# Performance work log

Measured on AMD Instinct MI355X. Metric: run time of the kernel, lower is better.

The kernel has to match this reference:

```python
import jax, jax.numpy as jnp
import numpy as np
from jax import lax

L, BSZ, H, W, U, P = 16, 8, 32, 32, 128, 256
KB = KC = KD = 3
NUM_GROUPS = 32
DT_MIN, DT_MAX = 1e-3, 1e-1
EPS = 1e-5


def setup_inputs() -> dict:
    key = jax.random.key(0)
    ks = jax.random.split(key, 10)
    return {
        "input_sequence": jax.random.normal(ks[0], (L, BSZ, H, W, U), jnp.float32),
        "x0": jax.random.normal(ks[1], (BSZ, H, W, P), jnp.float32),
        # negative real parts of continuous-time eigenvalues
        "Lambda_re": -(0.5 * jax.random.uniform(ks[2], (P,), jnp.float32) + 1e-2),
        "Lambda_im": jax.random.normal(ks[3], (P,), jnp.float32) * jnp.pi,
        # B param (P,U,kB,kB,2) real/imag stacked (he-normal scale)
        "B_ri": jax.random.normal(ks[4], (P, U, KB, KB, 2), jnp.float32) / np.sqrt(U * KB * KB),
        # C param (U,P,kC,kC,2) real/imag stacked
        "C_ri": jax.random.normal(ks[5], (U, P, KC, KC, 2), jnp.float32) / np.sqrt(P * KC * KC),
        "log_step": jax.random.uniform(ks[6], (P,), jnp.float32) * (np.log(DT_MAX) - np.log(DT_MIN)) + np.log(DT_MIN),
        # diagonal (depthwise) feedthrough D conv kernel, HWIO with I=1
        "D_kernel": jax.random.normal(ks[7], (KD, KD, 1, U), jnp.float32) / KD,
        "gn_scale": jnp.ones((U,), jnp.float32),
        "gn_bias": jnp.zeros((U,), jnp.float32),
    }


def _conv(x, k):
    # x: (N,H,W,Cin), k: (kh,kw,Cin,Cout), SAME padding, stride 1
    return lax.conv_general_dilated(x, k, (1, 1), 'SAME',
                                    dimension_numbers=('NHWC', 'HWIO', 'NHWC'))


def _group_norm(x, scale, bias):
    n, h, w, c = x.shape
    xg = x.reshape(n, h, w, NUM_GROUPS, c // NUM_GROUPS)
    mu = xg.mean(axis=(1, 2, 4), keepdims=True)
    var = xg.var(axis=(1, 2, 4), keepdims=True)
    xg = (xg - mu) * lax.rsqrt(var + EPS)
    return xg.reshape(n, h, w, c) * scale + bias


def reference(input_sequence, x0, Lambda_re, Lambda_im, B_ri, C_ri, log_step,
              D_kernel, gn_scale, gn_bias):
    # ---- discretization (faithful to source discretize_zoh: A_bar = Lambda*Delta, B_bar = Delta*B_tilde) ----
    Lam = jnp.minimum(Lambda_re, -1e-4) + 1j * Lambda_im      # clip_eigs, (P,) complex64
    step = jnp.exp(log_step)                                   # (P,)
    A_bar = Lam * step                                         # (P,) complex64
    # B_bar = (1/Lambda)*Lambda_bar*B_tilde = Delta * B_tilde, laid out HWIO (kB,kB,U,P)
    Bk_r = jnp.transpose(B_ri[..., 0] * step[:, None, None, None], (2, 3, 1, 0))
    Bk_i = jnp.transpose(B_ri[..., 1] * step[:, None, None, None], (2, 3, 1, 0))
    # C_tilde kernel HWIO (kC,kC,P,U)
    Ck_r = jnp.transpose(C_ri[..., 0], (2, 3, 1, 0))
    Ck_i = jnp.transpose(C_ri[..., 1], (2, 3, 1, 0))

    # ---- B (*) u for all timesteps (fold L into batch) ----
    u = input_sequence.reshape(L * BSZ, H, W, U)
    Bus = (_conv(u, Bk_r) + 1j * _conv(u, Bk_i)).reshape(L, BSZ, H, W, P)  # complex64
    Bus = Bus.at[0].add(A_bar * x0.astype(Bus.dtype))

    # ---- diagonal parallel scan: x_k = A * x_{k-1} + (B (*) u_k) ----
    A_elems = jnp.broadcast_to(A_bar[None, None, None, None, :], (L, 1, 1, 1, P))

    def binop(qi, qj):
        Ai, bi = qi
        Aj, bj = qj
        return Aj * Ai, Aj * bi + bj

    _, xs = lax.associative_scan(binop, (A_elems, Bus))        # xs: (L,BSZ,H,W,P) complex

    # ---- ys = 2*Re(C (*) x) ----
    xr = xs.real.reshape(L * BSZ, H, W, P)
    xi = xs.imag.reshape(L * BSZ, H, W, P)
    ys = 2.0 * (_conv(xr, Ck_r) - _conv(xi, Ck_i))             # (L*BSZ,H,W,U)

    # ---- C_D conv head ('standard' Diag_CD_Conv): diagonal D feedthrough + GroupNorm + act ----
    Du = lax.conv_general_dilated(u, D_kernel, (1, 1), 'SAME',
                                  dimension_numbers=('NHWC', 'HWIO', 'NHWC'),
                                  feature_group_count=U)
    h = jax.nn.gelu(_group_norm(ys + Du, gn_scale, gn_bias))
    ys_out = h.reshape(L, BSZ, H, W, U)

    x_last = xs[-1]                                            # (BSZ,H,W,P) complex
    x_last_ri = jnp.stack([x_last.real, x_last.imag], axis=-1) # real view for harness
    return x_last_ri, ys_out
```

## Files before the change

kernel.cpp:

```cpp
#include <hip/hip_runtime.h>
#include <hip/hip_bf16.h>
#include <math.h>

#define Ldim 16
#define BATCH 8
#define HWdim 1024

typedef __attribute__((ext_vector_type(8))) short s8v;
typedef __attribute__((ext_vector_type(4))) short s4v;
typedef __attribute__((ext_vector_type(2))) short s2v;
typedef __attribute__((ext_vector_type(4))) float f32x4;
typedef __attribute__((ext_vector_type(2))) float f32x2;

__device__ __forceinline__ short f2bf(float f) {
    __hip_bfloat16 h = __float2bfloat16(f);
    return __builtin_bit_cast(short, h);
}
__device__ __forceinline__ float bf2f(short s) {
    __hip_bfloat16 h = __builtin_bit_cast(__hip_bfloat16, s);
    return __bfloat162float(h);
}

__device__ __forceinline__ void gload_lds16(const short* g, short* l) {
    __builtin_amdgcn_global_load_lds(
        (const __attribute__((address_space(1))) void*)g,
        (__attribute__((address_space(3))) void*)l, 16, 0, 0);
}

__global__ __launch_bounds__(256)
void prep_kernel(const float* __restrict__ Lre, const float* __restrict__ Lim,
                 const float* __restrict__ B_ri, const float* __restrict__ C_ri,
                 const float* __restrict__ log_step, short* __restrict__ Wb,
                 short* __restrict__ Wc, float* __restrict__ Abar) {
    int tid = blockIdx.x * 256 + threadIdx.x;
    if (tid < 256) {
        float st = expf(log_step[tid]);
        Abar[tid] = fminf(Lre[tid], -1e-4f) * st;
        Abar[256 + tid] = Lim[tid] * st;
    }
    const int total = 9 * 512 * 128;
    for (int i = tid; i < total; i += gridDim.x * 256) {
        int tile = i >> 13;
        int r = i & 8191;
        int A = r * 2;
        int cout_lc = A >> 7;
        int remb = A & 127;
        int ci2 = remb ^ ((cout_lc & 7) << 4);
        int ci_local = ci2 >> 1;
        {
            int cgp = tile / 18;
            int rm = tile % 18;
            int ch = rm / 9, t = rm % 9;
            int cout = cgp * 128 + cout_lc;
            int p = cout >> 1, ri = cout & 1;
            int u = ch * 64 + ci_local;
            float val = B_ri[(((size_t)p * 128 + u) * 9 + t) * 2 + ri] * expf(log_step[p]);
            Wb[i] = f2bf(val);
        }
        {
            int ch = tile / 9;
            int t = tile % 9;
            int u = cout_lc;
            int k = ch * 64 + ci_local;
            int p = k >> 1, ri = k & 1;
            float val = C_ri[(((size_t)u * 256 + p) * 9 + t) * 2 + ri];
            val = ri ? -2.f * val : 2.f * val;
            Wc[i] = f2bf(val);
        }
    }
}

__global__ __launch_bounds__(256)
void ubf_slice_kernel(const float* __restrict__ u, short* __restrict__ Ubf,
                      int b0, int Gshift) {
    size_t t = (size_t)blockIdx.x * 256 + threadIdx.x;
    int c8 = (int)(t & 15);
    int hw = (int)(t >> 4) & 1023;
    int img = (int)(t >> 14);
    int l = img >> Gshift, bi = img & ((1 << Gshift) - 1);
    const float* src = u + (((size_t)(l * BATCH + b0 + bi) * HWdim + hw) * 128 + c8 * 8);
    f32x4 v0 = *(const f32x4*)src;
    f32x4 v1 = *(const f32x4*)(src + 4);
    s8v o;
#pragma unroll
    for (int j = 0; j < 4; ++j) { o[j] = f2bf(v0[j]); o[4 + j] = f2bf(v1[j]); }
    *(s8v*)(Ubf + ((size_t)img * HWdim + hw) * 128 + c8 * 8) = o;
}

template <int CIN, int COUT, bool INF32, bool INFULL, bool RMW>
__global__ __launch_bounds__(256, 2)
void conv_mfma(const void* __restrict__ inbuf, const short* __restrict__ Wt,
               short* __restrict__ outbuf, int b0, int Gshift) {
    constexpr int NCH = CIN / 64;
    constexpr int NT = NCH * 9;
    constexpr int NCGP = COUT / 128;
    __shared__ short ilds[6 * 34 * 64];
    __shared__ short wlds[3 * 8192];

    const int tid = threadIdx.x;
    const int lane = tid & 63;
    const int wv = tid >> 6;
    const int waveM = wv & 1, waveN = wv >> 1;
    const int lm = lane & 15, quad = lane >> 4;

    const int chunk = gridDim.x >> 3;
    const int wg = blockIdx.x;
    const int wgs = (wg & 7) * chunk + (wg >> 3);
    const int cgp = wgs % NCGP;
    const int h0 = (((wgs / NCGP) & 7)) * 4;
    const int img = wgs / (NCGP * 8);

    const int l = img >> Gshift;
    const int bi = img & ((1 << Gshift) - 1);
    const size_t inframe = INFULL ? (size_t)(l * BATCH + b0 + bi) : (size_t)img;

    constexpr int NST = 7;
    uint goff[NST];
    int laddr[NST];
#pragma unroll
    for (int j = 0; j < NST; ++j) {
        int idx = tid + j * 256;
        laddr[j] = -1;
        goff[j] = 0xFFFFFFFFu;
        if (idx < 6 * 34 * 8) {
            int cgi = idx & 7;
            int pos = idx >> 3;
            int w34 = pos % 34;
            int sr = pos / 34;
            int habs = h0 - 1 + sr, wabs = w34 - 1;
            laddr[j] = ((pos << 3) + (cgi ^ (pos & 7))) << 3;
            if ((unsigned)habs < 32u && (unsigned)wabs < 32u)
                goff[j] = (uint)(((uint)inframe * HWdim + habs * 32 + wabs) * CIN + cgi * 8);
        }
    }

    auto issue_W = [&](int j) {
        const short* src = Wt + ((size_t)cgp * NT + j) * 8192;
        short* dst = &wlds[(j % 3) * 8192];
#pragma unroll
        for (int r = 0; r < 4; ++r)
            gload_lds16(src + (size_t)(r * 256 + tid) * 8, dst + (r * 256 + wv * 64) * 8);
    };

    auto stage_input = [&](int ch) {
        s8v sreg[NST];
#pragma unroll
        for (int j = 0; j < NST; ++j) {
            s8v v = (s8v){0, 0, 0, 0, 0, 0, 0, 0};
            if (goff[j] != 0xFFFFFFFFu) {
                if constexpr (INF32) {
                    const float* src = (const float*)inbuf + goff[j] + ch * 64;
                    f32x4 a0 = *(const f32x4*)src;
                    f32x4 a1 = *(const f32x4*)(src + 4);
#pragma unroll
                    for (int q = 0; q < 4; ++q) { v[q] = f2bf(a0[q]); v[4 + q] = f2bf(a1[q]); }
                } else {
                    v = *(const s8v*)((const short*)inbuf + goff[j] + ch * 64);
                }
            }
            sreg[j] = v;
        }
#pragma unroll
        for (int j = 0; j < NST; ++j)
            if (laddr[j] >= 0) *(s8v*)&ilds[laddr[j]] = sreg[j];
    };

    f32x4 acc[4][4];
#pragma unroll
    for (int mt = 0; mt < 4; ++mt)
#pragma unroll
        for (int nt = 0; nt < 4; ++nt)
            acc[mt][nt] = (f32x4){0.f, 0.f, 0.f, 0.f};

    auto compute_tap = [&](int t, const short* wb) {
        int kh = t / 3, kw = t - kh * 3;
#pragma unroll
        for (int ks = 0; ks < 2; ++ks) {
            s8v a[4], b[4];
#pragma unroll
            for (int mt = 0; mt < 4; ++mt) {
                int p = (waveM * 2 + (mt >> 1) + kh) * 34 + (mt & 1) * 16 + lm + kw;
                int c = ks * 4 + quad;
                a[mt] = *(const s8v*)&ilds[(((p << 3) + (c ^ (p & 7))) << 3)];
            }
#pragma unroll
            for (int nt = 0; nt < 4; ++nt) {
                int cl = waveN * 64 + nt * 16 + lm;
                int ba = (cl * 128 + ks * 64 + quad * 16) ^ ((cl & 7) << 4);
                b[nt] = *(const s8v*)((const char*)wb + ba);
            }
            __builtin_amdgcn_s_setprio(1);
#pragma unroll
            for (int mt = 0; mt < 4; ++mt)
#pragma unroll
                for (int nt = 0; nt < 4; ++nt)
                    acc[mt][nt] = __builtin_amdgcn_mfma_f32_16x16x32_bf16(
                        b[nt], a[mt], acc[mt][nt], 0, 0, 0);
            __builtin_amdgcn_s_setprio(0);
        }
    };

    issue_W(0);
    if (NT > 1) issue_W(1);
    stage_input(0);
    asm volatile("s_waitcnt vmcnt(0) lgkmcnt(0)" ::: "memory");
    __builtin_amdgcn_sched_barrier(0);
    __builtin_amdgcn_s_barrier();

#pragma unroll
    for (int k = 0; k < NT; ++k) {
        const int ch = k / 9;
        const int t = k - ch * 9;
        if (k + 2 < NT) issue_W(k + 2);
        compute_tap(t, &wlds[(k % 3) * 8192]);
        if (k + 1 < NT) {
            if (k + 2 < NT) {
                asm volatile("s_waitcnt vmcnt(4)" ::: "memory");
            } else {
                asm volatile("s_waitcnt vmcnt(0)" ::: "memory");
            }
            __builtin_amdgcn_sched_barrier(0);
            __builtin_amdgcn_s_barrier();
            if (t == 8) {
                stage_input(ch + 1);
                asm volatile("s_waitcnt lgkmcnt(0)" ::: "memory");
                __builtin_amdgcn_sched_barrier(0);
                __builtin_amdgcn_s_barrier();
            }
        }
    }

#pragma unroll
    for (int mt = 0; mt < 4; ++mt) {
        int px = waveM * 64 + mt * 16 + lm;
        int r = px >> 5, w = px & 31;
        size_t rowbase = ((size_t)img * HWdim + (h0 + r) * 32 + w) * COUT +
                         cgp * 128 + waveN * 64 + quad * 4;
#pragma unroll
        for (int nt = 0; nt < 4; ++nt) {
            size_t oidx = rowbase + nt * 16;
            s4v o;
            if (RMW) {
                s4v old = *(const s4v*)&outbuf[oidx];
#pragma unroll
                for (int reg = 0; reg < 4; ++reg)
                    o[reg] = f2bf(acc[mt][nt][reg] + bf2f(old[reg]));
            } else {
#pragma unroll
                for (int reg = 0; reg < 4; ++reg)
                    o[reg] = f2bf(acc[mt][nt][reg]);
            }
            *(s4v*)&outbuf[oidx] = o;
        }
    }
}

__global__ __launch_bounds__(256)
void scan_kernel(const float* __restrict__ x0, const float* __restrict__ Abar,
                 short* __restrict__ X, float* __restrict__ out_xlast, int b0, int G) {
    int p = threadIdx.x;
    int hw = blockIdx.x;
    int bi = blockIdx.y;
    int b = b0 + bi;
    float Ar = Abar[p], Ai = Abar[256 + p];
    float xr = x0[((size_t)b * HWdim + hw) * 256 + p];
    float xi = 0.f;
    for (int l = 0; l < Ldim; ++l) {
        size_t base = ((size_t)(l * G + bi) * HWdim + hw) * 512 + p * 2;
        s2v v = *(s2v*)&X[base];
        float br = bf2f(v[0]), bim = bf2f(v[1]);
        float nr = Ar * xr - Ai * xi + br;
        float ni = Ar * xi + Ai * xr + bim;
        xr = nr; xi = ni;
        v[0] = f2bf(xr); v[1] = f2bf(xi);
        *(s2v*)&X[base] = v;
    }
    f32x2 o2 = {xr, xi};
    *(f32x2*)&out_xlast[(((size_t)b * HWdim + hw) * 256 + p) * 2] = o2;
}

template <bool UBF>
__global__ __launch_bounds__(256)
void du_kernel(const void* __restrict__ uin, const float* __restrict__ Dk,
               short* __restrict__ ys, int b0, int Gshift) {
    int tid = blockIdx.x * 256 + threadIdx.x;
    int c4 = tid & 31;
    int hw = (tid >> 5) & 1023;
    int img = tid >> 15;
    int h = hw >> 5, w = hw & 31;
    int l = img >> Gshift, bi = img & ((1 << Gshift) - 1);
    size_t fbase = UBF ? (size_t)img * HWdim * 128
                       : ((size_t)(l * BATCH + b0 + bi)) * HWdim * 128;
    float s0 = 0.f, s1 = 0.f, s2 = 0.f, s3 = 0.f;
#pragma unroll
    for (int kh = 0; kh < 3; ++kh)
#pragma unroll
        for (int kw = 0; kw < 3; ++kw) {
            int hh = h + kh - 1, wc = w + kw - 1;
            if ((unsigned)hh < 32u && (unsigned)wc < 32u) {
                f32x4 d = *(const f32x4*)&Dk[(kh * 3 + kw) * 128 + c4 * 4];
                size_t off = fbase + ((size_t)hh * 32 + wc) * 128 + c4 * 4;
                if (UBF) {
                    s4v v = *(const s4v*)((const short*)uin + off);
                    s0 += bf2f(v[0]) * d[0]; s1 += bf2f(v[1]) * d[1];
                    s2 += bf2f(v[2]) * d[2]; s3 += bf2f(v[3]) * d[3];
                } else {
                    f32x4 v = *(const f32x4*)((const float*)uin + off);
                    s0 += v[0] * d[0]; s1 += v[1] * d[1];
                    s2 += v[2] * d[2]; s3 += v[3] * d[3];
                }
            }
        }
    s4v o = {f2bf(s0), f2bf(s1), f2bf(s2), f2bf(s3)};
    *(s4v*)&ys[(size_t)tid * 4] = o;
}

__global__ __launch_bounds__(256)
void gnstats_kernel(const short* __restrict__ ys, float* __restrict__ stats) {
    int g = blockIdx.x;
    int img = blockIdx.y;
    int tid = threadIdx.x;
    float s = 0.f, s2 = 0.f;
    for (int hw = tid; hw < HWdim; hw += 256) {
        s4v v = *(const s4v*)&ys[((size_t)img * HWdim + hw) * 128 + g * 4];
#pragma unroll
        for (int j = 0; j < 4; ++j) {
            float f = bf2f(v[j]);
            s += f; s2 += f * f;
        }
    }
    __shared__ float red[16];
    for (int off = 32; off > 0; off >>= 1) {
        s += __shfl_down(s, off, 64);
        s2 += __shfl_down(s2, off, 64);
    }
    int wid = tid >> 6;
    if ((tid & 63) == 0) { red[wid] = s; red[8 + wid] = s2; }
    __syncthreads();
    if (tid == 0) {
        float S = 0.f, S2 = 0.f;
        for (int w2 = 0; w2 < 4; ++w2) { S += red[w2]; S2 += red[8 + w2]; }
        const float inv = 1.f / (HWdim * 4);
        float mean = S * inv;
        float var = S2 * inv - mean * mean;
        stats[(img * 32 + g) * 2 + 0] = mean;
        stats[(img * 32 + g) * 2 + 1] = var;
    }
}

__global__ __launch_bounds__(256)
void gnapply_kernel(const short* __restrict__ ys, const float* __restrict__ stats,
                    const float* __restrict__ scale, const float* __restrict__ bias,
                    float* __restrict__ out_ys, int b0, int Gshift) {
    int tid = blockIdx.x * 256 + threadIdx.x;
    int c4 = tid & 31;
    int hw = (tid >> 5) & 1023;
    int img = tid >> 15;
    int l = img >> Gshift, bi = img & ((1 << Gshift) - 1);
    float mean = stats[(img * 32 + c4) * 2 + 0];
    float var = stats[(img * 32 + c4) * 2 + 1];
    float rstd = rsqrtf(var + 1e-5f);
    s4v v = *(const s4v*)&ys[(size_t)tid * 4];
    f32x4 sc = *(const f32x4*)&scale[c4 * 4];
    f32x4 bs = *(const f32x4*)&bias[c4 * 4];
    f32x4 o;
    const float kAlpha = 0.7978845608028654f;
#pragma unroll
    for (int j = 0; j < 4; ++j) {
        float y = (bf2f(v[j]) - mean) * rstd * sc[j] + bs[j];
        float t = kAlpha * (y + 0.044715f * y * y * y);
        o[j] = 0.5f * y * (1.f + tanhf(t));
    }
    *(f32x4*)&out_ys[(((size_t)(l * BATCH + b0 + bi)) * HWdim + hw) * 128 + c4 * 4] = o;
}

extern "C" void kernel_launch(void* const* d_in, const int* in_sizes, int n_in,
                              void* d_out, int out_size, void* d_ws, size_t ws_size,
                              hipStream_t stream) {
    const float* useq = (const float*)d_in[0];
    const float* x0 = (const float*)d_in[1];
    const float* Lre = (const float*)d_in[2];
    const float* Lim = (const float*)d_in[3];
    const float* B_ri = (const float*)d_in[4];
    const float* C_ri = (const float*)d_in[5];
    const float* log_step = (const float*)d_in[6];
    const float* Dk = (const float*)d_in[7];
    const float* gsc = (const float*)d_in[8];
    const float* gbi = (const float*)d_in[9];
    float* out = (float*)d_out;

    const size_t WBYTES = 9 * 512 * 128 * 2;

    int G = 2;
    bool ubf = false;
    {
        auto need = [&](int g, bool u) -> size_t {
            size_t base = 2 * WBYTES + 2048 + (size_t)g * 4096;
            size_t x = (size_t)g * Ldim * HWdim * 512 * 2;
            size_t ysb = (size_t)g * Ldim * HWdim * 128 * 2;
            size_t ub = (size_t)g * Ldim * HWdim * 128 * 2;
            return base + x + ysb + (u ? ub : 0);
        };
        if (ws_size >= need(8, true)) { G = 8; ubf = true; }
        else if (ws_size >= need(8, false)) { G = 8; }
        else if (ws_size >= need(4, true)) { G = 4; ubf = true; }
        else if (ws_size >= need(4, false)) { G = 4; }
        else if (ws_size >= need(2, true)) { G = 2; ubf = true; }
    }
    int Gshift = (G == 8) ? 3 : (G == 4) ? 2 : 1;
    int imgs = Ldim * G;

    char* wsb = (char*)d_ws;
    short* Wb = (short*)(wsb);
    short* Wc = (short*)(wsb + WBYTES);
    float* Abar = (float*)(wsb + 2 * WBYTES);
    float* stats = (float*)(wsb + 2 * WBYTES + 2048);
    size_t offX = 2 * WBYTES + 2048 + (size_t)G * 4096;
    short* X = (short*)(wsb + offX);
    size_t offYS = offX + (size_t)G * Ldim * HWdim * 512 * 2;
    short* YS = (short*)(wsb + offYS);
    short* Ubf = (short*)(wsb + offYS + (size_t)G * Ldim * HWdim * 128 * 2);

    prep_kernel<<<2304, 256, 0, stream>>>(Lre, Lim, B_ri, C_ri, log_step, Wb, Wc, Abar);

    for (int b0 = 0; b0 < BATCH; b0 += G) {
        if (ubf) {
            ubf_slice_kernel<<<imgs * 64, 256, 0, stream>>>(useq, Ubf, b0, Gshift);
            conv_mfma<128, 512, false, false, false><<<8 * 4 * imgs, 256, 0, stream>>>(
                Ubf, Wb, X, b0, Gshift);
        } else {
            conv_mfma<128, 512, true, true, false><<<8 * 4 * imgs, 256, 0, stream>>>(
                useq, Wb, X, b0, Gshift);
        }
        scan_kernel<<<dim3(HWdim, G), 256, 0, stream>>>(x0, Abar, X, out, b0, G);
        if (ubf)
            du_kernel<true><<<imgs * 128, 256, 0, stream>>>(Ubf, Dk, YS, b0, Gshift);
        else
            du_kernel<false><<<imgs * 128, 256, 0, stream>>>(useq, Dk, YS, b0, Gshift);
        conv_mfma<512, 128, false, false, true><<<8 * imgs, 256, 0, stream>>>(
            X, Wc, YS, b0, Gshift);
        gnstats_kernel<<<dim3(32, imgs), 256, 0, stream>>>(YS, stats);
        gnapply_kernel<<<imgs * 128, 256, 0, stream>>>(YS, stats, gsc, gbi, out + 4194304, b0,
                                                       Gshift);
    }
}
```

Baseline: 609.6 us.

## Split weight tiles into K-halves, templatize row tile, nontemporal stores

Repacks the B and C conv weights into half-size tiles, one per 32-channel K-step, so the LDS weight ring is halved and the pipeline advances per K-half. The conv kernel gains a row-tile template parameter. The C conv (512->128) now uses 2-row tiles with twice as many workgroups, and launch bounds rise to 3 waves per SIMD for higher occupancy. Nontemporal loads and stores are added in the scan, the conv output and the GN apply to reduce cache pollution. The trade-off is more barriers per tap and lower reuse per tile in the C conv.

```diff
diff --git a/kernel.cpp b/kernel.cpp
--- a/kernel.cpp
+++ b/kernel.cpp
@@ -40,28 +40,29 @@
     }
     const int total = 9 * 512 * 128;
     for (int i = tid; i < total; i += gridDim.x * 256) {
-        int tile = i >> 13;
-        int r = i & 8191;
-        int A = r * 2;
-        int cout_lc = A >> 7;
-        int remb = A & 127;
-        int ci2 = remb ^ ((cout_lc & 7) << 4);
-        int ci_local = ci2 >> 1;
+        int j = i >> 12;
+        int L = (i & 4095) * 2;
+        int c1 = L >> 7;
+        int c0 = ((L >> 6) ^ (L >> 8)) & 1;
+        int cout_lc = c1 * 2 + c0;
+        int cih = ((L ^ ((cout_lc & 7) << 4)) >> 1) & 31;
+        int ks = j & 1;
+        int tt = j >> 1;
         {
-            int cgp = tile / 18;
-            int rm = tile % 18;
+            int cgp = tt / 18;
+            int rm = tt % 18;
             int ch = rm / 9, t = rm % 9;
             int cout = cgp * 128 + cout_lc;
             int p = cout >> 1, ri = cout & 1;
-            int u = ch * 64 + ci_local;
+            int u = ch * 64 + ks * 32 + cih;
             float val = B_ri[(((size_t)p * 128 + u) * 9 + t) * 2 + ri] * expf(log_step[p]);
             Wb[i] = f2bf(val);
         }
         {
-            int ch = tile / 9;
-            int t = tile % 9;
+            int ch = tt / 9;
+            int t = tt % 9;
             int u = cout_lc;
-            int k = ch * 64 + ci_local;
+            int k = ch * 64 + ks * 32 + cih;
             int p = k >> 1, ri = k & 1;
             float val = C_ri[(((size_t)u * 256 + p) * 9 + t) * 2 + ri];
             val = ri ? -2.f * val : 2.f * val;
@@ -87,15 +88,18 @@
     *(s8v*)(Ubf + ((size_t)img * HWdim + hw) * 128 + c8 * 8) = o;
 }
 
-template <int CIN, int COUT, bool INF32, bool INFULL, bool RMW>
-__global__ __launch_bounds__(256, 2)
+template <int TM, int CIN, int COUT, bool INF32, bool INFULL, bool RMW>
+__global__ __launch_bounds__(256, 3)
 void conv_mfma(const void* __restrict__ inbuf, const short* __restrict__ Wt,
                short* __restrict__ outbuf, int b0, int Gshift) {
     constexpr int NCH = CIN / 64;
     constexpr int NT = NCH * 9;
     constexpr int NCGP = COUT / 128;
-    __shared__ short ilds[6 * 34 * 64];
-    __shared__ short wlds[3 * 8192];
+    constexpr int NRG = 32 / TM;
+    constexpr int PR = TM + 2;
+    constexpr int NST = (PR * 34 * 8 + 255) / 256;
+    __shared__ short ilds[PR * 34 * 64];
+    __shared__ short wlds[3 * 4096];
 
     const int tid = threadIdx.x;
     const int lane = tid & 63;
@@ -107,14 +111,13 @@
     const int wg = blockIdx.x;
     const int wgs = (wg & 7) * chunk + (wg >> 3);
     const int cgp = wgs % NCGP;
-    const int h0 = (((wgs / NCGP) & 7)) * 4;
-    const int img = wgs / (NCGP * 8);
+    const int h0 = ((wgs / NCGP) % NRG) * TM;
+    const int img = wgs / (NCGP * NRG);
 
     const int l = img >> Gshift;
     const int bi = img & ((1 << Gshift) - 1);
     const size_t inframe = INFULL ? (size_t)(l * BATCH + b0 + bi) : (size_t)img;
 
-    constexpr int NST = 7;
     uint goff[NST];
     int laddr[NST];
 #pragma unroll
@@ -122,7 +125,7 @@
         int idx = tid + j * 256;
         laddr[j] = -1;
         goff[j] = 0xFFFFFFFFu;
-        if (idx < 6 * 34 * 8) {
+        if (idx < PR * 34 * 8) {
             int cgi = idx & 7;
             int pos = idx >> 3;
             int w34 = pos % 34;
@@ -134,11 +137,11 @@
         }
     }
 
-    auto issue_W = [&](int j) {
-        const short* src = Wt + ((size_t)cgp * NT + j) * 8192;
-        short* dst = &wlds[(j % 3) * 8192];
-#pragma unroll
-        for (int r = 0; r < 4; ++r)
+    auto issue_half = [&](int j, int slot) {
+        const short* src = Wt + ((size_t)cgp * (2 * NT) + j) * 4096;
+        short* dst = &wlds[slot * 4096];
+#pragma unroll
+        for (int r = 0; r < 2; ++r)
             gload_lds16(src + (size_t)(r * 256 + tid) * 8, dst + (r * 256 + wv * 64) * 8);
     };
 
@@ -165,74 +168,80 @@
             if (laddr[j] >= 0) *(s8v*)&ilds[laddr[j]] = sreg[j];
     };
 
-    f32x4 acc[4][4];
-#pragma unroll
-    for (int mt = 0; mt < 4; ++mt)
+    f32x4 acc[TM][4];
+#pragma unroll
+    for (int mt = 0; mt < TM; ++mt)
 #pragma unroll
         for (int nt = 0; nt < 4; ++nt)
             acc[mt][nt] = (f32x4){0.f, 0.f, 0.f, 0.f};
 
-    auto compute_tap = [&](int t, const short* wb) {
-        int kh = t / 3, kw = t - kh * 3;
-#pragma unroll
-        for (int ks = 0; ks < 2; ++ks) {
-            s8v a[4], b[4];
-#pragma unroll
-            for (int mt = 0; mt < 4; ++mt) {
-                int p = (waveM * 2 + (mt >> 1) + kh) * 34 + (mt & 1) * 16 + lm + kw;
-                int c = ks * 4 + quad;
-                a[mt] = *(const s8v*)&ilds[(((p << 3) + (c ^ (p & 7))) << 3)];
-            }
-#pragma unroll
-            for (int nt = 0; nt < 4; ++nt) {
-                int cl = waveN * 64 + nt * 16 + lm;
-                int ba = (cl * 128 + ks * 64 + quad * 16) ^ ((cl & 7) << 4);
-                b[nt] = *(const s8v*)((const char*)wb + ba);
-            }
-            __builtin_amdgcn_s_setprio(1);
-#pragma unroll
-            for (int mt = 0; mt < 4; ++mt)
-#pragma unroll
-                for (int nt = 0; nt < 4; ++nt)
-                    acc[mt][nt] = __builtin_amdgcn_mfma_f32_16x16x32_bf16(
-                        b[nt], a[mt], acc[mt][nt], 0, 0, 0);
-            __builtin_amdgcn_s_setprio(0);
-        }
+    auto compute_ks = [&](int kh, int kw, int ks, int slot) {
+        const char* wb = (const char*)wlds + slot * 8192;
+        s8v a[TM], b[4];
+#pragma unroll
+        for (int mt = 0; mt < TM; ++mt) {
+            int pxb = waveM * (TM * 16) + mt * 16;
+            int p = ((pxb >> 5) + kh) * 34 + (pxb & 31) + lm + kw;
+            int c = ks * 4 + quad;
+            a[mt] = *(const s8v*)&ilds[(((p << 3) + (c ^ (p & 7))) << 3)];
+        }
+#pragma unroll
+        for (int nt = 0; nt < 4; ++nt) {
+            int cl = waveN * 64 + nt * 16 + lm;
+            int ba = (cl * 64 + quad * 16) ^ ((cl & 7) << 4);
+            b[nt] = *(const s8v*)(wb + ba);
+        }
+        __builtin_amdgcn_s_setprio(1);
+#pragma unroll
+        for (int mt = 0; mt < TM; ++mt)
+#pragma unroll
+            for (int nt = 0; nt < 4; ++nt)
+                acc[mt][nt] = __builtin_amdgcn_mfma_f32_16x16x32_bf16(
+                    b[nt], a[mt], acc[mt][nt], 0, 0, 0);
+        __builtin_amdgcn_s_setprio(0);
     };
 
-    issue_W(0);
-    if (NT > 1) issue_W(1);
+    issue_half(0, 0);
+    issue_half(1, 1);
     stage_input(0);
     asm volatile("s_waitcnt vmcnt(0) lgkmcnt(0)" ::: "memory");
     __builtin_amdgcn_sched_barrier(0);
     __builtin_amdgcn_s_barrier();
 
-#pragma unroll
-    for (int k = 0; k < NT; ++k) {
-        const int ch = k / 9;
-        const int t = k - ch * 9;
-        if (k + 2 < NT) issue_W(k + 2);
-        compute_tap(t, &wlds[(k % 3) * 8192]);
-        if (k + 1 < NT) {
-            if (k + 2 < NT) {
-                asm volatile("s_waitcnt vmcnt(4)" ::: "memory");
-            } else {
-                asm volatile("s_waitcnt vmcnt(0)" ::: "memory");
+#pragma unroll 1
+    for (int ch = 0; ch < NCH; ++ch) {
+#pragma unroll
+        for (int t = 0; t < 9; ++t) {
+            const int kh = t / 3, kw = t - kh * 3;
+#pragma unroll
+            for (int ks = 0; ks < 2; ++ks) {
+                const int ls = t * 2 + ks;
+                const int jg = ch * 18 + ls + 2;
+                if (jg < 2 * NT) issue_half(jg, (ls + 2) % 3);
+                compute_ks(kh, kw, ks, ls % 3);
+                const bool last = (ch == NCH - 1) && (ls == 17);
+                if (!last) {
+                    if (jg < 2 * NT) {
+                        asm volatile("s_waitcnt vmcnt(2)" ::: "memory");
+                    } else {
+                        asm volatile("s_waitcnt vmcnt(0)" ::: "memory");
+                    }
+                    __builtin_amdgcn_sched_barrier(0);
+                    __builtin_amdgcn_s_barrier();
+                    if (ls == 17) {
+                        stage_input(ch + 1);
+                        asm volatile("s_waitcnt lgkmcnt(0)" ::: "memory");
+                        __builtin_amdgcn_sched_barrier(0);
+                        __builtin_amdgcn_s_barrier();
+                    }
+                }
             }
-            __builtin_amdgcn_sched_barrier(0);
-            __builtin_amdgcn_s_barrier();
-            if (t == 8) {
-                stage_input(ch + 1);
-                asm volatile("s_waitcnt lgkmcnt(0)" ::: "memory");
-                __builtin_amdgcn_sched_barrier(0);
-                __builtin_amdgcn_s_barrier();
-            }
-        }
-    }
-
-#pragma unroll
-    for (int mt = 0; mt < 4; ++mt) {
-        int px = waveM * 64 + mt * 16 + lm;
+        }
+    }
+
+#pragma unroll
+    for (int mt = 0; mt < TM; ++mt) {
+        int px = waveM * (TM * 16) + mt * 16 + lm;
         int r = px >> 5, w = px & 31;
         size_t rowbase = ((size_t)img * HWdim + (h0 + r) * 32 + w) * COUT +
                          cgp * 128 + waveN * 64 + quad * 4;
@@ -245,12 +254,13 @@
 #pragma unroll
                 for (int reg = 0; reg < 4; ++reg)
                     o[reg] = f2bf(acc[mt][nt][reg] + bf2f(old[reg]));
+                *(s4v*)&outbuf[oidx] = o;
             } else {
 #pragma unroll
                 for (int reg = 0; reg < 4; ++reg)
                     o[reg] = f2bf(acc[mt][nt][reg]);
+                __builtin_nontemporal_store(o, (s4v*)&outbuf[oidx]);
             }
-            *(s4v*)&outbuf[oidx] = o;
         }
     }
 }
@@ -267,7 +277,7 @@
     float xi = 0.f;
     for (int l = 0; l < Ldim; ++l) {
         size_t base = ((size_t)(l * G + bi) * HWdim + hw) * 512 + p * 2;
-        s2v v = *(s2v*)&X[base];
+        s2v v = __builtin_nontemporal_load((const s2v*)&X[base]);
         float br = bf2f(v[0]), bim = bf2f(v[1]);
         float nr = Ar * xr - Ai * xi + br;
         float ni = Ar * xi + Ai * xr + bim;
@@ -276,7 +286,7 @@
         *(s2v*)&X[base] = v;
     }
     f32x2 o2 = {xr, xi};
-    *(f32x2*)&out_xlast[(((size_t)b * HWdim + hw) * 256 + p) * 2] = o2;
+    __builtin_nontemporal_store(o2, (f32x2*)&out_xlast[(((size_t)b * HWdim + hw) * 256 + p) * 2]);
 }
 
 template <bool UBF>
@@ -371,7 +381,8 @@
         float t = kAlpha * (y + 0.044715f * y * y * y);
         o[j] = 0.5f * y * (1.f + tanhf(t));
     }
-    *(f32x4*)&out_ys[(((size_t)(l * BATCH + b0 + bi)) * HWdim + hw) * 128 + c4 * 4] = o;
+    __builtin_nontemporal_store(
+        o, (f32x4*)&out_ys[(((size_t)(l * BATCH + b0 + bi)) * HWdim + hw) * 128 + c4 * 4]);
 }
 
 extern "C" void kernel_launch(void* const* d_in, const int* in_sizes, int n_in,
@@ -426,10 +437,10 @@
     for (int b0 = 0; b0 < BATCH; b0 += G) {
         if (ubf) {
             ubf_slice_kernel<<<imgs * 64, 256, 0, stream>>>(useq, Ubf, b0, Gshift);
-            conv_mfma<128, 512, false, false, false><<<8 * 4 * imgs, 256, 0, stream>>>(
+            conv_mfma<4, 128, 512, false, false, false><<<8 * 4 * imgs, 256, 0, stream>>>(
                 Ubf, Wb, X, b0, Gshift);
         } else {
-            conv_mfma<128, 512, true, true, false><<<8 * 4 * imgs, 256, 0, stream>>>(
+            conv_mfma<4, 128, 512, true, true, false><<<8 * 4 * imgs, 256, 0, stream>>>(
                 useq, Wb, X, b0, Gshift);
         }
         scan_kernel<<<dim3(HWdim, G), 256, 0, stream>>>(x0, Abar, X, out, b0, G);
@@ -437,7 +448,7 @@
             du_kernel<true><<<imgs * 128, 256, 0, stream>>>(Ubf, Dk, YS, b0, Gshift);
         else
             du_kernel<false><<<imgs * 128, 256, 0, stream>>>(useq, Dk, YS, b0, Gshift);
-        conv_mfma<512, 128, false, false, true><<<8 * imgs, 256, 0, stream>>>(
+        conv_mfma<2, 512, 128, false, false, true><<<16 * imgs, 256, 0, stream>>>(
             X, Wc, YS, b0, Gshift);
         gnstats_kernel<<<dim3(32, imgs), 256, 0, stream>>>(YS, stats);
         gnapply_kernel<<<imgs * 128, 256, 0, stream>>>(YS, stats, gsc, gbi, out + 4194304, b0,
```

After: 750.2 us. 1.23x slower.
